# Performance work log

Hardware: AMD Instinct MI355X
Metric: run time of the kernel (lower is better)

## Reference

```python
import jax, jax.numpy as jnp
import numpy as np

E, H, I, T = 8, 1024, 2816, 8192  # experts, hidden, intermediate, total tokens


def setup_inputs() -> dict:
    key = jax.random.key(0)
    k1, k2, k3, k4 = jax.random.split(key, 4)
    x = jax.random.normal(k1, (T, H), dtype=jnp.float32)
    # xavier_normal std = sqrt(2 / (fan_in + fan_out))
    std = (2.0 / (H + I)) ** 0.5
    gate = jax.random.normal(k2, (E, H, I), dtype=jnp.float32) * std
    up = jax.random.normal(k3, (E, H, I), dtype=jnp.float32) * std
    down = jax.random.normal(k4, (E, I, H), dtype=jnp.float32) * std
    # tokens are pre-permuted so each expert's tokens are contiguous; equal split here
    tokens_per_expert = jnp.full((E,), T // E, dtype=jnp.int32)
    return {
        "permuted_local_hidden_states": x,
        "grouped_gate_proj": gate,
        "grouped_up_proj": up,
        "grouped_down_proj": down,
        "tokens_per_expert": tokens_per_expert,
    }


def reference(permuted_local_hidden_states, grouped_gate_proj, grouped_up_proj,
              grouped_down_proj, tokens_per_expert):
    # grouped GEMM: for expert e, rows in its contiguous segment are multiplied by W[e]
    o1 = jax.lax.ragged_dot(permuted_local_hidden_states, grouped_gate_proj,
                            tokens_per_expert)            # [T, I]
    o2 = jax.lax.ragged_dot(permuted_local_hidden_states, grouped_up_proj,
                            tokens_per_expert)            # [T, I]
    inter = jax.nn.silu(o1) * o2                          # SwiGLU  [T, I]
    out = jax.lax.ragged_dot(inter, grouped_down_proj, tokens_per_expert)  # [T, H]
    return out
```

## Files before the change

### kernel.cpp

```cpp
#include <hip/hip_runtime.h>
#include <hip/hip_bf16.h>


#define E_ 8
#define H_ 1024
#define I_ 2816
#define T_ 8192

typedef unsigned short u16;
typedef __attribute__((ext_vector_type(8))) short s16x8;
typedef __attribute__((ext_vector_type(8))) unsigned short u16x8;
typedef __attribute__((ext_vector_type(4))) float f32x4;

__device__ __forceinline__ void async16(const u16* g, u16* l) {
  __builtin_amdgcn_global_load_lds((__attribute__((address_space(1))) void*)g,
                                   (__attribute__((address_space(3))) void*)l, 16, 0, 0);
}

__device__ __forceinline__ u16 f2b(float f) {
  union { __hip_bfloat16 h; u16 u; } c;
  c.h = __float2bfloat16(f);
  return c.u;
}

__global__ __launch_bounds__(256) void convx_k(const float* __restrict__ x,
                                               u16* __restrict__ xb) {
  size_t i = ((size_t)blockIdx.x * 256 + threadIdx.x) * 8;
  float4 v0 = *(const float4*)(x + i);
  float4 v1 = *(const float4*)(x + i + 4);
  u16x8 b;
  b[0] = f2b(v0.x); b[1] = f2b(v0.y); b[2] = f2b(v0.z); b[3] = f2b(v0.w);
  b[4] = f2b(v1.x); b[5] = f2b(v1.y); b[6] = f2b(v1.z); b[7] = f2b(v1.w);
  *(u16x8*)(xb + i) = b;
}

template <int R, int C>
__device__ __forceinline__ void tconv_tile(const float* __restrict__ in,
                                           u16* __restrict__ out,
                                           int bx, int by, int t) {
  __shared__ u16 lt[64 * 64];
  const int c0 = bx * 64, r0 = by * 64;

  const int rl = (t >> 3) * 2;
  const int cl = (t & 7) * 8;
  const float* p = in + (size_t)(r0 + rl) * C + (c0 + cl);
  float4 v0 = *(const float4*)(p);
  float4 v1 = *(const float4*)(p + 4);
  float4 v2 = *(const float4*)(p + C);
  float4 v3 = *(const float4*)(p + C + 4);

  float lo[8] = {v0.x, v0.y, v0.z, v0.w, v1.x, v1.y, v1.z, v1.w};
  float hi[8] = {v2.x, v2.y, v2.z, v2.w, v3.x, v3.y, v3.z, v3.w};
  const int chunk = ((rl >> 3) ^ (cl >> 3)) << 3;
  u16* wp = lt + cl * 64 + chunk + (rl & 7);
#pragma unroll
  for (int j = 0; j < 8; ++j) {
    unsigned pk = (unsigned)f2b(lo[j]) | ((unsigned)f2b(hi[j]) << 16);
    *(unsigned*)(wp + j * 64) = pk;
  }
  __syncthreads();

  const int c = t >> 2;
  const int rs = (t & 3) * 16;
  const int rc = rs >> 3;
  u16x8 o0 = *(const u16x8*)(lt + c * 64 + ((rc ^ (c >> 3)) << 3));
  u16x8 o1 = *(const u16x8*)(lt + c * 64 + (((rc + 1) ^ (c >> 3)) << 3));
  u16* op = out + (size_t)(c0 + c) * R + (r0 + rs);
  *(u16x8*)(op) = o0;
  *(u16x8*)(op + 8) = o1;
}

__global__ __launch_bounds__(256) void tconvGU_k(const float* __restrict__ G,
                                                 const float* __restrict__ U,
                                                 u16* __restrict__ GT,
                                                 u16* __restrict__ UT) {
  const int z = blockIdx.z;
  const size_t eoff = (size_t)(z >> 1) * (size_t)H_ * I_;
  const float* in = ((z & 1) ? U : G) + eoff;
  u16* out = ((z & 1) ? UT : GT) + eoff;
  tconv_tile<H_, I_>(in, out, blockIdx.x, blockIdx.y, threadIdx.x);
}

__global__ __launch_bounds__(256) void tconvD_k(const float* __restrict__ D,
                                                u16* __restrict__ DT) {
  const size_t eoff = (size_t)blockIdx.z * (size_t)H_ * I_;
  tconv_tile<I_, H_>(D + eoff, DT + eoff, blockIdx.x, blockIdx.y, threadIdx.x);
}

__global__ __launch_bounds__(256, 2) void gemm12_k(
    const u16* __restrict__ X, const u16* __restrict__ GT,
    const u16* __restrict__ UT, const int* __restrict__ tpe,
    u16* __restrict__ inter) {
  __shared__ u16 sA[128 * 64];
  __shared__ u16 sG[64 * 64];
  __shared__ u16 sU[64 * 64];
  const int t = threadIdx.x;
  const int m0 = blockIdx.y * 128;
  const int n0 = blockIdx.x * 64;

  int e = 0, seg_end = T_;
  {
    int s = 0;
    for (int i = 0; i < E_; ++i) {
      int c = tpe[i];
      if (m0 < s + c) { e = i; seg_end = s + c; break; }
      s += c;
    }
  }
  const u16* GTe = GT + (size_t)e * I_ * H_;
  const u16* UTe = UT + (size_t)e * I_ * H_;

  const int sj = ((t & 7) ^ ((t >> 3) & 7)) * 8;
  const u16* gA = X + (size_t)(m0 + (t >> 3)) * H_ + sj;
  const u16* gG = GTe + (size_t)(n0 + (t >> 3)) * H_ + sj;
  const u16* gU = UTe + (size_t)(n0 + (t >> 3)) * H_ + sj;
  u16* lA = sA + t * 8;
  u16* lG = sG + t * 8;
  u16* lU = sU + t * 8;

  const int l = t & 63, w = t >> 6;
  const int wm = (w & 1) * 64, wn = (w >> 1) * 32;
  const int c0 = (((l >> 4) ^ (l & 7))) * 8;
  const u16* fA = sA + (size_t)(wm + (l & 15)) * 64;
  const u16* fG = sG + (size_t)(wn + (l & 15)) * 64;
  const u16* fU = sU + (size_t)(wn + (l & 15)) * 64;

  f32x4 accG[4][2], accU[4][2];
#pragma unroll
  for (int mi = 0; mi < 4; ++mi)
#pragma unroll
    for (int ni = 0; ni < 2; ++ni) {
      accG[mi][ni] = (f32x4){0.f, 0.f, 0.f, 0.f};
      accU[mi][ni] = (f32x4){0.f, 0.f, 0.f, 0.f};
    }

  for (int k0 = 0; k0 < H_; k0 += 64) {
    async16(gA + k0, lA);
    async16(gA + 32 * H_ + k0, lA + 2048);
    async16(gA + 64 * H_ + k0, lA + 4096);
    async16(gA + 96 * H_ + k0, lA + 6144);
    async16(gG + k0, lG);
    async16(gG + 32 * H_ + k0, lG + 2048);
    async16(gU + k0, lU);
    async16(gU + 32 * H_ + k0, lU + 2048);
    __syncthreads();
#pragma unroll
    for (int ks = 0; ks < 2; ++ks) {
      const int co = c0 ^ (ks * 32);
      s16x8 aF[4], gF[2], uF[2];
#pragma unroll
      for (int mi = 0; mi < 4; ++mi) aF[mi] = *(const s16x8*)(fA + mi * 1024 + co);
#pragma unroll
      for (int ni = 0; ni < 2; ++ni) {
        gF[ni] = *(const s16x8*)(fG + ni * 1024 + co);
        uF[ni] = *(const s16x8*)(fU + ni * 1024 + co);
      }
#pragma unroll
      for (int mi = 0; mi < 4; ++mi)
#pragma unroll
        for (int ni = 0; ni < 2; ++ni) {
          accG[mi][ni] = __builtin_amdgcn_mfma_f32_16x16x32_bf16(aF[mi], gF[ni], accG[mi][ni], 0, 0, 0);
          accU[mi][ni] = __builtin_amdgcn_mfma_f32_16x16x32_bf16(aF[mi], uF[ni], accU[mi][ni], 0, 0, 0);
        }
    }
    __syncthreads();
  }

  const int colb = l & 15, rowb = (l >> 4) * 4;
#pragma unroll
  for (int mi = 0; mi < 4; ++mi)
#pragma unroll
    for (int ni = 0; ni < 2; ++ni) {
      const size_t gcol = (size_t)(n0 + wn + ni * 16 + colb);
#pragma unroll
      for (int r = 0; r < 4; ++r) {
        int grow = m0 + wm + mi * 16 + rowb + r;
        if (grow < seg_end) {
          float o1 = accG[mi][ni][r];
          float o2 = accU[mi][ni][r];
          float sv = o1 / (1.f + __expf(-o1));
          inter[(size_t)grow * I_ + gcol] = f2b(sv * o2);
        }
      }
    }
}

__global__ __launch_bounds__(256, 2) void gemm3_k(
    const u16* __restrict__ A, const u16* __restrict__ DT,
    const int* __restrict__ tpe, float* __restrict__ out) {
  __shared__ u16 sA[128 * 64];
  __shared__ u16 sB[128 * 64];
  const int t = threadIdx.x;
  const int m0 = blockIdx.y * 128;
  const int n0 = blockIdx.x * 128;

  int e = 0, seg_end = T_;
  {
    int s = 0;
    for (int i = 0; i < E_; ++i) {
      int c = tpe[i];
      if (m0 < s + c) { e = i; seg_end = s + c; break; }
      s += c;
    }
  }
  const u16* DTe = DT + (size_t)e * H_ * I_;

  const int sj = ((t & 7) ^ ((t >> 3) & 7)) * 8;
  const u16* gA = A + (size_t)(m0 + (t >> 3)) * I_ + sj;
  const u16* gB = DTe + (size_t)(n0 + (t >> 3)) * I_ + sj;
  u16* lA = sA + t * 8;
  u16* lB = sB + t * 8;

  const int l = t & 63, w = t >> 6;
  const int wm = (w & 1) * 64, wn = (w >> 1) * 64;
  const int c0 = (((l >> 4) ^ (l & 7))) * 8;
  const u16* fA = sA + (size_t)(wm + (l & 15)) * 64;
  const u16* fB = sB + (size_t)(wn + (l & 15)) * 64;

  f32x4 acc[4][4];
#pragma unroll
  for (int mi = 0; mi < 4; ++mi)
#pragma unroll
    for (int ni = 0; ni < 4; ++ni) acc[mi][ni] = (f32x4){0.f, 0.f, 0.f, 0.f};

  for (int k0 = 0; k0 < I_; k0 += 64) {
    async16(gA + k0, lA);
    async16(gA + 32 * I_ + k0, lA + 2048);
    async16(gA + 64 * I_ + k0, lA + 4096);
    async16(gA + 96 * I_ + k0, lA + 6144);
    async16(gB + k0, lB);
    async16(gB + 32 * I_ + k0, lB + 2048);
    async16(gB + 64 * I_ + k0, lB + 4096);
    async16(gB + 96 * I_ + k0, lB + 6144);
    __syncthreads();
#pragma unroll
    for (int ks = 0; ks < 2; ++ks) {
      const int co = c0 ^ (ks * 32);
      s16x8 aF[4], bF[4];
#pragma unroll
      for (int mi = 0; mi < 4; ++mi) aF[mi] = *(const s16x8*)(fA + mi * 1024 + co);
#pragma unroll
      for (int ni = 0; ni < 4; ++ni) bF[ni] = *(const s16x8*)(fB + ni * 1024 + co);
#pragma unroll
      for (int mi = 0; mi < 4; ++mi)
#pragma unroll
        for (int ni = 0; ni < 4; ++ni)
          acc[mi][ni] = __builtin_amdgcn_mfma_f32_16x16x32_bf16(aF[mi], bF[ni], acc[mi][ni], 0, 0, 0);
    }
    __syncthreads();
  }

  const int colb = l & 15, rowb = (l >> 4) * 4;
#pragma unroll
  for (int mi = 0; mi < 4; ++mi)
#pragma unroll
    for (int ni = 0; ni < 4; ++ni) {
      const size_t gcol = (size_t)(n0 + wn + ni * 16 + colb);
#pragma unroll
      for (int r = 0; r < 4; ++r) {
        int grow = m0 + wm + mi * 16 + rowb + r;
        if (grow < seg_end) out[(size_t)grow * H_ + gcol] = acc[mi][ni][r];
      }
    }
}

extern "C" void kernel_launch(void* const* d_in, const int* in_sizes, int n_in,
                              void* d_out, int out_size, void* d_ws, size_t ws_size,
                              hipStream_t stream) {
  const float* X = (const float*)d_in[0];
  const float* G = (const float*)d_in[1];
  const float* U = (const float*)d_in[2];
  const float* D = (const float*)d_in[3];
  const int* tpe = (const int*)d_in[4];
  float* out = (float*)d_out;

  const size_t W = (size_t)E_ * H_ * I_;
  if (ws_size < 3 * W * sizeof(u16)) return;
  u16* r0 = (u16*)d_ws;
  u16* r1 = r0 + W;
  u16* r2 = r1 + W;
  u16* xb = (u16*)d_out;

  convx_k<<<dim3((T_ * H_) / (256 * 8)), 256, 0, stream>>>(X, xb);
  tconvGU_k<<<dim3(I_ / 64, H_ / 64, E_ * 2), 256, 0, stream>>>(G, U, r0, r1);
  gemm12_k<<<dim3(I_ / 64, T_ / 128), 256, 0, stream>>>(xb, r0, r1, tpe, r2);
  tconvD_k<<<dim3(H_ / 64, I_ / 64, E_), 256, 0, stream>>>(D, r0);
  gemm3_k<<<dim3(H_ / 128, T_ / 128), 256, 0, stream>>>(r2, r0, tpe, out);
}
```

Measured before the change: 464.0 us.

## Double-buffer down-proj GEMM, merge X/GU conversion kernels, padded transpose tile

The down-projection GEMM gets two LDS buffers so the async global-to-LDS loads for the next K tile are issued before computing the current one, with one barrier per iteration. The X bf16 conversion and the gate/up transpose-convert are merged into one launch to save launch overhead and let both jobs share the GPU. The transpose tile switches from an XOR swizzle to a padded 68-stride layout with 4x4 per-thread blocks. Double buffering doubles LDS use in gemm3, which may lower occupancy. The prefetch also appears to race with the wait: there is no explicit wait on the async loads before the barrier.

```diff
diff --git a/kernel.cpp b/kernel.cpp
--- a/kernel.cpp
+++ b/kernel.cpp
@@ -8,6 +8,7 @@
 #define T_ 8192
 
 typedef unsigned short u16;
+typedef __attribute__((ext_vector_type(4))) unsigned short u16x4;
 typedef __attribute__((ext_vector_type(8))) short s16x8;
 typedef __attribute__((ext_vector_type(8))) unsigned short u16x8;
 typedef __attribute__((ext_vector_type(4))) float f32x4;
@@ -23,62 +24,71 @@
   return c.u;
 }
 
-__global__ __launch_bounds__(256) void convx_k(const float* __restrict__ x,
-                                               u16* __restrict__ xb) {
-  size_t i = ((size_t)blockIdx.x * 256 + threadIdx.x) * 8;
-  float4 v0 = *(const float4*)(x + i);
-  float4 v1 = *(const float4*)(x + i + 4);
-  u16x8 b;
-  b[0] = f2b(v0.x); b[1] = f2b(v0.y); b[2] = f2b(v0.z); b[3] = f2b(v0.w);
-  b[4] = f2b(v1.x); b[5] = f2b(v1.y); b[6] = f2b(v1.z); b[7] = f2b(v1.w);
-  *(u16x8*)(xb + i) = b;
-}
-
 template <int R, int C>
 __device__ __forceinline__ void tconv_tile(const float* __restrict__ in,
                                            u16* __restrict__ out,
                                            int bx, int by, int t) {
-  __shared__ u16 lt[64 * 64];
+  __shared__ u16 lt[64 * 68];
   const int c0 = bx * 64, r0 = by * 64;
 
-  const int rl = (t >> 3) * 2;
-  const int cl = (t & 7) * 8;
-  const float* p = in + (size_t)(r0 + rl) * C + (c0 + cl);
-  float4 v0 = *(const float4*)(p);
-  float4 v1 = *(const float4*)(p + 4);
-  float4 v2 = *(const float4*)(p + C);
-  float4 v3 = *(const float4*)(p + C + 4);
-
-  float lo[8] = {v0.x, v0.y, v0.z, v0.w, v1.x, v1.y, v1.z, v1.w};
-  float hi[8] = {v2.x, v2.y, v2.z, v2.w, v3.x, v3.y, v3.z, v3.w};
-  const int chunk = ((rl >> 3) ^ (cl >> 3)) << 3;
-  u16* wp = lt + cl * 64 + chunk + (rl & 7);
-#pragma unroll
-  for (int j = 0; j < 8; ++j) {
-    unsigned pk = (unsigned)f2b(lo[j]) | ((unsigned)f2b(hi[j]) << 16);
-    *(unsigned*)(wp + j * 64) = pk;
+  const int cQ = (t & 15) * 4;
+  const int rB = (t >> 4) * 4;
+  const float* p = in + (size_t)(r0 + rB) * C + (c0 + cQ);
+  float4 v[4];
+#pragma unroll
+  for (int j = 0; j < 4; ++j) v[j] = *(const float4*)(p + (size_t)j * C);
+  const float* vf = (const float*)v;
+#pragma unroll
+  for (int q = 0; q < 4; ++q) {
+    u16x4 w;
+    w[0] = f2b(vf[0 * 4 + q]);
+    w[1] = f2b(vf[1 * 4 + q]);
+    w[2] = f2b(vf[2 * 4 + q]);
+    w[3] = f2b(vf[3 * 4 + q]);
+    *(u16x4*)(lt + (cQ + q) * 68 + rB) = w;
   }
   __syncthreads();
 
   const int c = t >> 2;
   const int rs = (t & 3) * 16;
-  const int rc = rs >> 3;
-  u16x8 o0 = *(const u16x8*)(lt + c * 64 + ((rc ^ (c >> 3)) << 3));
-  u16x8 o1 = *(const u16x8*)(lt + c * 64 + (((rc + 1) ^ (c >> 3)) << 3));
+  const u16* rp = lt + c * 68 + rs;
+  u16x4 b0 = *(const u16x4*)(rp);
+  u16x4 b1 = *(const u16x4*)(rp + 4);
+  u16x4 b2 = *(const u16x4*)(rp + 8);
+  u16x4 b3 = *(const u16x4*)(rp + 12);
+  u16x8 o0 = __builtin_shufflevector(b0, b1, 0, 1, 2, 3, 4, 5, 6, 7);
+  u16x8 o1 = __builtin_shufflevector(b2, b3, 0, 1, 2, 3, 4, 5, 6, 7);
   u16* op = out + (size_t)(c0 + c) * R + (r0 + rs);
   *(u16x8*)(op) = o0;
   *(u16x8*)(op + 8) = o1;
 }
 
-__global__ __launch_bounds__(256) void tconvGU_k(const float* __restrict__ G,
-                                                 const float* __restrict__ U,
-                                                 u16* __restrict__ GT,
-                                                 u16* __restrict__ UT) {
-  const int z = blockIdx.z;
-  const size_t eoff = (size_t)(z >> 1) * (size_t)H_ * I_;
-  const float* in = ((z & 1) ? U : G) + eoff;
-  u16* out = ((z & 1) ? UT : GT) + eoff;
-  tconv_tile<H_, I_>(in, out, blockIdx.x, blockIdx.y, threadIdx.x);
+__global__ __launch_bounds__(256) void prep_k(const float* __restrict__ X,
+                                              const float* __restrict__ G,
+                                              const float* __restrict__ U,
+                                              u16* __restrict__ xb,
+                                              u16* __restrict__ GT,
+                                              u16* __restrict__ UT) {
+  const int bid = blockIdx.x;
+  const int t = threadIdx.x;
+  if (bid < 4096) {
+    size_t i = ((size_t)bid * 256 + t) * 8;
+    float4 v0 = *(const float4*)(X + i);
+    float4 v1 = *(const float4*)(X + i + 4);
+    u16x8 b;
+    b[0] = f2b(v0.x); b[1] = f2b(v0.y); b[2] = f2b(v0.z); b[3] = f2b(v0.w);
+    b[4] = f2b(v1.x); b[5] = f2b(v1.y); b[6] = f2b(v1.z); b[7] = f2b(v1.w);
+    *(u16x8*)(xb + i) = b;
+  } else {
+    int b = bid - 4096;
+    const int bx = b % 44; b /= 44;
+    const int by = b % 16; b /= 16;
+    const int z = b;
+    const size_t eoff = (size_t)(z >> 1) * (size_t)H_ * I_;
+    const float* in = ((z & 1) ? U : G) + eoff;
+    u16* out = ((z & 1) ? UT : GT) + eoff;
+    tconv_tile<H_, I_>(in, out, bx, by, t);
+  }
 }
 
 __global__ __launch_bounds__(256) void tconvD_k(const float* __restrict__ D,
@@ -188,8 +198,8 @@
 __global__ __launch_bounds__(256, 2) void gemm3_k(
     const u16* __restrict__ A, const u16* __restrict__ DT,
     const int* __restrict__ tpe, float* __restrict__ out) {
-  __shared__ u16 sA[128 * 64];
-  __shared__ u16 sB[128 * 64];
+  __shared__ u16 sA[2][128 * 64];
+  __shared__ u16 sB[2][128 * 64];
   const int t = threadIdx.x;
   const int m0 = blockIdx.y * 128;
   const int n0 = blockIdx.x * 128;
@@ -208,14 +218,13 @@
   const int sj = ((t & 7) ^ ((t >> 3) & 7)) * 8;
   const u16* gA = A + (size_t)(m0 + (t >> 3)) * I_ + sj;
   const u16* gB = DTe + (size_t)(n0 + (t >> 3)) * I_ + sj;
-  u16* lA = sA + t * 8;
-  u16* lB = sB + t * 8;
+  const int toff = t * 8;
 
   const int l = t & 63, w = t >> 6;
   const int wm = (w & 1) * 64, wn = (w >> 1) * 64;
   const int c0 = (((l >> 4) ^ (l & 7))) * 8;
-  const u16* fA = sA + (size_t)(wm + (l & 15)) * 64;
-  const u16* fB = sB + (size_t)(wn + (l & 15)) * 64;
+  const int foff = (wm + (l & 15)) * 64;
+  const int goff = (wn + (l & 15)) * 64;
 
   f32x4 acc[4][4];
 #pragma unroll
@@ -223,16 +232,27 @@
 #pragma unroll
     for (int ni = 0; ni < 4; ++ni) acc[mi][ni] = (f32x4){0.f, 0.f, 0.f, 0.f};
 
+#define STAGE3(buf, k0)                                   \
+  {                                                       \
+    u16* dA = &sA[buf][0] + toff;                         \
+    u16* dB = &sB[buf][0] + toff;                         \
+    async16(gA + (k0), dA);                               \
+    async16(gA + 32 * I_ + (k0), dA + 2048);              \
+    async16(gA + 64 * I_ + (k0), dA + 4096);              \
+    async16(gA + 96 * I_ + (k0), dA + 6144);              \
+    async16(gB + (k0), dB);                               \
+    async16(gB + 32 * I_ + (k0), dB + 2048);              \
+    async16(gB + 64 * I_ + (k0), dB + 4096);              \
+    async16(gB + 96 * I_ + (k0), dB + 6144);              \
+  }
+
+  STAGE3(0, 0);
+  __syncthreads();
+  int cur = 0;
   for (int k0 = 0; k0 < I_; k0 += 64) {
-    async16(gA + k0, lA);
-    async16(gA + 32 * I_ + k0, lA + 2048);
-    async16(gA + 64 * I_ + k0, lA + 4096);
-    async16(gA + 96 * I_ + k0, lA + 6144);
-    async16(gB + k0, lB);
-    async16(gB + 32 * I_ + k0, lB + 2048);
-    async16(gB + 64 * I_ + k0, lB + 4096);
-    async16(gB + 96 * I_ + k0, lB + 6144);
-    __syncthreads();
+    if (k0 + 64 < I_) STAGE3(cur ^ 1, k0 + 64);
+    const u16* fA = &sA[cur][0] + foff;
+    const u16* fB = &sB[cur][0] + goff;
 #pragma unroll
     for (int ks = 0; ks < 2; ++ks) {
       const int co = c0 ^ (ks * 32);
@@ -248,7 +268,9 @@
           acc[mi][ni] = __builtin_amdgcn_mfma_f32_16x16x32_bf16(aF[mi], bF[ni], acc[mi][ni], 0, 0, 0);
     }
     __syncthreads();
-  }
+    cur ^= 1;
+  }
+#undef STAGE3
 
   const int colb = l & 15, rowb = (l >> 4) * 4;
 #pragma unroll
@@ -281,8 +303,7 @@
   u16* r2 = r1 + W;
   u16* xb = (u16*)d_out;
 
-  convx_k<<<dim3((T_ * H_) / (256 * 8)), 256, 0, stream>>>(X, xb);
-  tconvGU_k<<<dim3(I_ / 64, H_ / 64, E_ * 2), 256, 0, stream>>>(G, U, r0, r1);
+  prep_k<<<dim3(4096 + 11264), 256, 0, stream>>>(X, G, U, xb, r0, r1);
   gemm12_k<<<dim3(I_ / 64, T_ / 128), 256, 0, stream>>>(xb, r0, r1, tpe, r2);
   tconvD_k<<<dim3(H_ / 64, I_ / 64, E_), 256, 0, stream>>>(D, r0);
   gemm3_k<<<dim3(H_ / 128, T_ / 128), 256, 0, stream>>>(r2, r0, tpe, out);
```

Measured after the change: 456.8 us. About the same (-1.5%).
